# Kernel tuning notes

Measured on AMD Instinct MI355X. Metric: run time of the kernel, lower is better.

Reference implementation:

```python
import jax, jax.numpy as jnp
import numpy as np


def setup_inputs() -> dict:
    key = jax.random.key(0)
    kq, kk, kv = jax.random.split(key, 3)
    B, N, D = 16, 2048, 64
    queries = jax.random.normal(kq, (B, N, D), dtype=jnp.float32)
    keys = jax.random.normal(kk, (B, N, D), dtype=jnp.float32)
    values = jax.random.normal(kv, (B, N, D), dtype=jnp.float32)
    return {"queries": queries, "keys": keys, "values": values}


def reference(queries, keys, values):
    d = queries.shape[-1]
    scale = 1.0 / jnp.sqrt(jnp.asarray(d, dtype=queries.dtype))
    # scores: [B, Nq, Nk]
    scores = jnp.einsum("bqd,bkd->bqk", queries, keys) * scale
    # Faithful to the original: softmax over dim=0 (the batch dimension).
    attn = jax.nn.softmax(scores, axis=0)
    # dropout p=0.0 -> identity
    return jnp.einsum("bqk,bkd->bqd", attn, values)
```

## Files before the change

### kernel.cpp

```cpp
#include <hip/hip_runtime.h>
#include <hip/hip_bf16.h>

typedef __attribute__((ext_vector_type(8))) short short8;
typedef __attribute__((ext_vector_type(4))) short short4v;
typedef __attribute__((ext_vector_type(2))) int   int2v;
typedef __attribute__((ext_vector_type(4))) float floatx4;

#define BATCH 16
#define SEQ   2048
#define DIM   64
#define QSCALE 0.18033688011112042f
#define WS_NEED (12u*1024u*1024u)

__device__ __forceinline__ unsigned short f2bf(float f) {
    return __builtin_bit_cast(unsigned short, __float2bfloat16(f));
}

#if defined(__has_builtin)
#if __has_builtin(__builtin_amdgcn_exp2f)
#define EXP2(x) __builtin_amdgcn_exp2f(x)
#endif
#endif
#ifndef EXP2
#define EXP2(x) exp2f(x)
#endif

#if defined(__has_builtin)
#if __has_builtin(__builtin_amdgcn_mfma_f32_16x16x16bf16_1k)
#define MFMA16(A,B,C) __builtin_amdgcn_mfma_f32_16x16x16bf16_1k(A,B,C,0,0,0)
#elif __has_builtin(__builtin_amdgcn_mfma_f32_16x16x16_bf16)
#define MFMA16(A,B,C) __builtin_amdgcn_mfma_f32_16x16x16_bf16(A,B,C,0,0,0)
#endif
#endif
#ifndef MFMA16
__device__ __forceinline__ floatx4 mfma16_asm(short4v a, short4v b, floatx4 c) {
    asm volatile("s_nop 1\n\tv_mfma_f32_16x16x16_bf16 %0, %1, %2, %0"
                 : "+v"(c) : "v"(a), "v"(b));
    return c;
}
#define MFMA16(A,B,C) mfma16_asm(A,B,C)
#endif

__global__ __launch_bounds__(256)
void convert_kernel(const float* __restrict__ Q, const float* __restrict__ K,
                    const float* __restrict__ V, unsigned short* __restrict__ ws) {
    const int t = blockIdx.x * 256 + threadIdx.x;
    if (t < 524288) {
        const int region = t >> 18;
        const int r = t & 262143;
        const int b = r >> 14;
        const int rem = r & 16383;
        const int t16 = rem >> 7;
        const int st  = (rem >> 6) & 1;
        const int l   = rem & 63;
        const int a = l & 15, g = l >> 4;
        const float* src = (region == 0 ? Q : K) +
            ((size_t)(b * SEQ + t16 * 16 + a)) * DIM + st * 32 + g * 8;
        const float s = (region == 0) ? QSCALE : 1.0f;
        short8 o;
        #pragma unroll
        for (int p = 0; p < 8; ++p) o[p] = (short)f2bf(src[p] * s);
        *(short8*)(ws + (size_t)region * 2097152 + (size_t)r * 8) = o;
    } else {
        const int r = t - 524288;
        const int b  = r >> 13;
        const int kt = (r >> 6) & 127;
        const int l  = r & 63;
        const int a = l & 15, g = l >> 4;
        const float* src = V + ((size_t)(b * SEQ + kt * 16 + g * 4)) * DIM + a;
        short8 o0, o1;
        #pragma unroll
        for (int dt = 0; dt < 2; ++dt)
            #pragma unroll
            for (int p = 0; p < 4; ++p)
                o0[dt * 4 + p] = (short)f2bf(src[(size_t)p * DIM + dt * 16]);
        #pragma unroll
        for (int dt = 2; dt < 4; ++dt)
            #pragma unroll
            for (int p = 0; p < 4; ++p)
                o1[(dt - 2) * 4 + p] = (short)f2bf(src[(size_t)p * DIM + dt * 16]);
        unsigned short* dst = ws + 4194304 + (size_t)r * 16;
        *(short8*)(dst)     = o0;
        *(short8*)(dst + 8) = o1;
    }
}

__global__ __launch_bounds__(512)
void dpa_main(const unsigned short* __restrict__ Qw, const unsigned short* __restrict__ Kw,
              const unsigned short* __restrict__ Vw, float* __restrict__ Og) {
    __shared__ __align__(16) float dl[2][4][64][8];

    const int tid = threadIdx.x;
    const int l = tid & 63;
    const int w = tid >> 6;
    const int a = l & 15, g = l >> 4;
    const int bx = blockIdx.x;
    const int ch = bx & 3;
    const int qt = bx >> 2;
    const int b0 = w * 2;
    const int wsw = w ^ (l >> 3);

    const unsigned short* Kb = Kw + (size_t)b0 * 131072 + l * 8;
    const unsigned short* Vb = Vw + (size_t)b0 * 131072 + l * 16;

    short8 Qf[2][2];
    {
        const unsigned short* Qb = Qw + (size_t)b0 * 131072 + qt * 1024 + l * 8;
        #pragma unroll
        for (int bb = 0; bb < 2; ++bb)
            #pragma unroll
            for (int st = 0; st < 2; ++st)
                Qf[bb][st] = *(const short8*)(Qb + bb * 131072 + st * 512);
    }

    short8 Kf[2][2];
    #pragma unroll
    for (int bb = 0; bb < 2; ++bb)
        #pragma unroll
        for (int st = 0; st < 2; ++st)
            Kf[bb][st] = *(const short8*)(Kb + bb * 131072 + (ch * 32) * 1024 + st * 512);

    floatx4 O[2][4];
    #pragma unroll
    for (int bb = 0; bb < 2; ++bb)
        #pragma unroll
        for (int dt = 0; dt < 4; ++dt) O[bb][dt] = (floatx4)0.0f;

    #pragma unroll 2
    for (int it = 0; it < 32; ++it) {
        const int buf = it & 1;
        const int kt = ch * 32 + it;

        floatx4 S[2];
        __builtin_amdgcn_s_setprio(1);
        #pragma unroll
        for (int bb = 0; bb < 2; ++bb) {
            floatx4 s = (floatx4)0.0f;
            s = __builtin_amdgcn_mfma_f32_16x16x32_bf16(Kf[bb][0], Qf[bb][0], s, 0, 0, 0);
            s = __builtin_amdgcn_mfma_f32_16x16x32_bf16(Kf[bb][1], Qf[bb][1], s, 0, 0, 0);
            S[bb] = s;
        }
        __builtin_amdgcn_s_setprio(0);

        const int ktn = (it < 31) ? (kt + 1) : kt;
        #pragma unroll
        for (int bb = 0; bb < 2; ++bb)
            #pragma unroll
            for (int st = 0; st < 2; ++st)
                Kf[bb][st] = *(const short8*)(Kb + bb * 131072 + ktn * 1024 + st * 512);

        short8 V01[2], V23[2];
        #pragma unroll
        for (int bb = 0; bb < 2; ++bb) {
            const unsigned short* vp = Vb + bb * 131072 + kt * 1024;
            V01[bb] = *(const short8*)(vp);
            V23[bb] = *(const short8*)(vp + 8);
        }

        #pragma unroll
        for (int r = 0; r < 4; ++r) {
            float e0 = EXP2(S[0][r]);
            float e1 = EXP2(S[1][r]);
            S[0][r] = e0; S[1][r] = e1;
            dl[buf][r][l][wsw] = e0 + e1;
        }
        __syncthreads();

        float fr[4];
        #pragma unroll
        for (int r = 0; r < 4; ++r) {
            const floatx4 t0 = *(const floatx4*)&dl[buf][r][l][0];
            const floatx4 t1 = *(const floatx4*)&dl[buf][r][l][4];
            const floatx4 ts = t0 + t1;
            fr[r] = __builtin_amdgcn_rcpf((ts[0] + ts[1]) + (ts[2] + ts[3]));
        }

        #pragma unroll
        for (int bb = 0; bb < 2; ++bb) {
            const unsigned int c0 = __builtin_bit_cast(unsigned int, S[bb][0] * fr[0]) + 0x8000u;
            const unsigned int c1 = __builtin_bit_cast(unsigned int, S[bb][1] * fr[1]) + 0x8000u;
            const unsigned int c2 = __builtin_bit_cast(unsigned int, S[bb][2] * fr[2]) + 0x8000u;
            const unsigned int c3 = __builtin_bit_cast(unsigned int, S[bb][3] * fr[3]) + 0x8000u;
            int2v pp;
            pp[0] = (int)__builtin_amdgcn_perm(c1, c0, 0x07060302u);
            pp[1] = (int)__builtin_amdgcn_perm(c3, c2, 0x07060302u);
            const short4v af = __builtin_bit_cast(short4v, pp);

            const short4v vb0 = __builtin_shufflevector(V01[bb], V01[bb], 0, 1, 2, 3);
            const short4v vb1 = __builtin_shufflevector(V01[bb], V01[bb], 4, 5, 6, 7);
            const short4v vb2 = __builtin_shufflevector(V23[bb], V23[bb], 0, 1, 2, 3);
            const short4v vb3 = __builtin_shufflevector(V23[bb], V23[bb], 4, 5, 6, 7);

            __builtin_amdgcn_s_setprio(1);
            O[bb][0] = MFMA16(af, vb0, O[bb][0]);
            O[bb][1] = MFMA16(af, vb1, O[bb][1]);
            O[bb][2] = MFMA16(af, vb2, O[bb][2]);
            O[bb][3] = MFMA16(af, vb3, O[bb][3]);
            __builtin_amdgcn_s_setprio(0);
        }
    }

    asm volatile("s_nop 7\n\ts_nop 7" :::);

    #pragma unroll
    for (int bb = 0; bb < 2; ++bb)
        #pragma unroll
        for (int dt = 0; dt < 4; ++dt)
            #pragma unroll
            for (int r = 0; r < 4; ++r)
                unsafeAtomicAdd(Og + ((size_t)((b0 + bb) * SEQ + qt * 16 + g * 4 + r)) * DIM
                                    + dt * 16 + a,
                                O[bb][dt][r]);
}

__global__ __launch_bounds__(512)
void dpa_naive(const float* __restrict__ Q, const float* __restrict__ K,
               const float* __restrict__ V, float* __restrict__ out) {
    __shared__ float attn_lds[BATCH][8][64];
    const int tid = threadIdx.x;
    const int lane_k = tid & 63, row_q = tid >> 6, lane_d = tid & 63;
    const int q0 = blockIdx.x * 8;
    float acc[BATCH];
    #pragma unroll
    for (int b = 0; b < BATCH; ++b) acc[b] = 0.0f;
    for (int k0 = 0; k0 < SEQ; k0 += 64) {
        float s[BATCH];
        #pragma unroll
        for (int b = 0; b < BATCH; ++b) {
            const float4* qrow = (const float4*)(Q + ((size_t)b * SEQ + (q0 + row_q)) * DIM);
            const float4* krow = (const float4*)(K + ((size_t)b * SEQ + (k0 + lane_k)) * DIM);
            float a0 = 0.f;
            #pragma unroll
            for (int d4 = 0; d4 < 16; ++d4) {
                float4 qa = qrow[d4]; float4 kb = krow[d4];
                a0 += qa.x*kb.x + qa.y*kb.y + qa.z*kb.z + qa.w*kb.w;
            }
            s[b] = a0 * 0.125f;
        }
        float m = s[0];
        #pragma unroll
        for (int b = 1; b < BATCH; ++b) m = fmaxf(m, s[b]);
        float den = 0.f;
        #pragma unroll
        for (int b = 0; b < BATCH; ++b) { s[b] = __expf(s[b] - m); den += s[b]; }
        const float inv = 1.0f / den;
        #pragma unroll
        for (int b = 0; b < BATCH; ++b) attn_lds[b][row_q][lane_k] = s[b] * inv;
        __syncthreads();
        #pragma unroll
        for (int b = 0; b < BATCH; ++b) {
            const float* vbase = V + ((size_t)b * SEQ + k0) * DIM + lane_d;
            float acc2 = 0.f;
            #pragma unroll 8
            for (int kk = 0; kk < 64; ++kk) acc2 += attn_lds[b][row_q][kk] * vbase[(size_t)kk * DIM];
            acc[b] += acc2;
        }
        __syncthreads();
    }
    #pragma unroll
    for (int b = 0; b < BATCH; ++b)
        out[((size_t)b * SEQ + (q0 + row_q)) * DIM + lane_d] = acc[b];
}

extern "C" void kernel_launch(void* const* d_in, const int* in_sizes, int n_in,
                              void* d_out, int out_size, void* d_ws, size_t ws_size,
                              hipStream_t stream) {
    const float* Q = (const float*)d_in[0];
    const float* K = (const float*)d_in[1];
    const float* V = (const float*)d_in[2];
    float* out = (float*)d_out;

    if (ws_size < WS_NEED) {
        dpa_naive<<<dim3(SEQ / 8), dim3(512), 0, stream>>>(Q, K, V, out);
        return;
    }
    unsigned short* ws = (unsigned short*)d_ws;
    hipMemsetAsync(d_out, 0, (size_t)out_size * sizeof(float), stream);
    convert_kernel<<<dim3(2560), dim3(256), 0, stream>>>(Q, K, V, ws);
    dpa_main<<<dim3(512), dim3(512), 0, stream>>>(ws, ws + 2097152, ws + 4194304, out);
}
```

Baseline: 81.93 us.

## Software-pipeline QK/exp of next key tile with PV of previous tile

Restructures the main attention loop into a skewed pipeline. Each step computes QK scores and exponentials for key tile T while the batch-softmax normalisation and PV MFMAs for tile T-1 run in the same step, with tile T-1's V loads issued early. The aim is to hide MFMA and exp latency behind each other and give the V loads more time to land. In exchange the loop now needs two __syncthreads per iteration instead of one to protect the double-buffered LDS partial sums. The LDS row stride is also padded from 8 to 12 floats, which is meant to reduce bank conflicts.

Result: no change. 82.31 us (+0.5%).

```diff
diff --git a/kernel.cpp b/kernel.cpp
--- a/kernel.cpp
+++ b/kernel.cpp
@@ -24,6 +24,8 @@
 #ifndef EXP2
 #define EXP2(x) exp2f(x)
 #endif
+
+#define MFMA32(A,B,C) __builtin_amdgcn_mfma_f32_16x16x32_bf16(A,B,C,0,0,0)
 
 #if defined(__has_builtin)
 #if __has_builtin(__builtin_amdgcn_mfma_f32_16x16x16bf16_1k)
@@ -88,7 +90,7 @@
 __global__ __launch_bounds__(512)
 void dpa_main(const unsigned short* __restrict__ Qw, const unsigned short* __restrict__ Kw,
               const unsigned short* __restrict__ Vw, float* __restrict__ Og) {
-    __shared__ __align__(16) float dl[2][4][64][8];
+    __shared__ __align__(16) float dl[2][4][64][12];
 
     const int tid = threadIdx.x;
     const int l = tid & 63;
@@ -126,78 +128,103 @@
         #pragma unroll
         for (int dt = 0; dt < 4; ++dt) O[bb][dt] = (floatx4)0.0f;
 
-    #pragma unroll 2
-    for (int it = 0; it < 32; ++it) {
-        const int buf = it & 1;
-        const int kt = ch * 32 + it;
-
-        floatx4 S[2];
-        __builtin_amdgcn_s_setprio(1);
-        #pragma unroll
-        for (int bb = 0; bb < 2; ++bb) {
-            floatx4 s = (floatx4)0.0f;
-            s = __builtin_amdgcn_mfma_f32_16x16x32_bf16(Kf[bb][0], Qf[bb][0], s, 0, 0, 0);
-            s = __builtin_amdgcn_mfma_f32_16x16x32_bf16(Kf[bb][1], Qf[bb][1], s, 0, 0, 0);
-            S[bb] = s;
-        }
-        __builtin_amdgcn_s_setprio(0);
-
-        const int ktn = (it < 31) ? (kt + 1) : kt;
-        #pragma unroll
-        for (int bb = 0; bb < 2; ++bb)
-            #pragma unroll
-            for (int st = 0; st < 2; ++st)
-                Kf[bb][st] = *(const short8*)(Kb + bb * 131072 + ktn * 1024 + st * 512);
-
-        short8 V01[2], V23[2];
-        #pragma unroll
-        for (int bb = 0; bb < 2; ++bb) {
-            const unsigned short* vp = Vb + bb * 131072 + kt * 1024;
-            V01[bb] = *(const short8*)(vp);
-            V23[bb] = *(const short8*)(vp + 8);
-        }
-
-        #pragma unroll
-        for (int r = 0; r < 4; ++r) {
-            float e0 = EXP2(S[0][r]);
-            float e1 = EXP2(S[1][r]);
-            S[0][r] = e0; S[1][r] = e1;
-            dl[buf][r][l][wsw] = e0 + e1;
-        }
-        __syncthreads();
-
-        float fr[4];
-        #pragma unroll
-        for (int r = 0; r < 4; ++r) {
-            const floatx4 t0 = *(const floatx4*)&dl[buf][r][l][0];
-            const floatx4 t1 = *(const floatx4*)&dl[buf][r][l][4];
-            const floatx4 ts = t0 + t1;
-            fr[r] = __builtin_amdgcn_rcpf((ts[0] + ts[1]) + (ts[2] + ts[3]));
-        }
-
-        #pragma unroll
-        for (int bb = 0; bb < 2; ++bb) {
-            const unsigned int c0 = __builtin_bit_cast(unsigned int, S[bb][0] * fr[0]) + 0x8000u;
-            const unsigned int c1 = __builtin_bit_cast(unsigned int, S[bb][1] * fr[1]) + 0x8000u;
-            const unsigned int c2 = __builtin_bit_cast(unsigned int, S[bb][2] * fr[2]) + 0x8000u;
-            const unsigned int c3 = __builtin_bit_cast(unsigned int, S[bb][3] * fr[3]) + 0x8000u;
-            int2v pp;
-            pp[0] = (int)__builtin_amdgcn_perm(c1, c0, 0x07060302u);
-            pp[1] = (int)__builtin_amdgcn_perm(c3, c2, 0x07060302u);
-            const short4v af = __builtin_bit_cast(short4v, pp);
-
-            const short4v vb0 = __builtin_shufflevector(V01[bb], V01[bb], 0, 1, 2, 3);
-            const short4v vb1 = __builtin_shufflevector(V01[bb], V01[bb], 4, 5, 6, 7);
-            const short4v vb2 = __builtin_shufflevector(V23[bb], V23[bb], 0, 1, 2, 3);
-            const short4v vb3 = __builtin_shufflevector(V23[bb], V23[bb], 4, 5, 6, 7);
-
-            __builtin_amdgcn_s_setprio(1);
-            O[bb][0] = MFMA16(af, vb0, O[bb][0]);
-            O[bb][1] = MFMA16(af, vb1, O[bb][1]);
-            O[bb][2] = MFMA16(af, vb2, O[bb][2]);
-            O[bb][3] = MFMA16(af, vb3, O[bb][3]);
-            __builtin_amdgcn_s_setprio(0);
-        }
+    floatx4 SA[2], SB[2];
+
+#define QKEXP(T, SOUT)                                                        \
+    __builtin_amdgcn_s_setprio(1);                                            \
+    {                                                                         \
+        floatx4 s0 = (floatx4)0.0f, s1 = (floatx4)0.0f;                       \
+        s0 = MFMA32(Kf[0][0], Qf[0][0], s0);                                  \
+        s0 = MFMA32(Kf[0][1], Qf[0][1], s0);                                  \
+        s1 = MFMA32(Kf[1][0], Qf[1][0], s1);                                  \
+        s1 = MFMA32(Kf[1][1], Qf[1][1], s1);                                  \
+        SOUT[0] = s0; SOUT[1] = s1;                                           \
+    }                                                                         \
+    __builtin_amdgcn_s_setprio(0);                                            \
+    {                                                                         \
+        const int ktn_ = ch * 32 + (((T) < 31) ? (T) + 1 : 31);               \
+        Kf[0][0] = *(const short8*)(Kb + 0 * 131072 + ktn_ * 1024);           \
+        Kf[0][1] = *(const short8*)(Kb + 0 * 131072 + ktn_ * 1024 + 512);     \
+        Kf[1][0] = *(const short8*)(Kb + 1 * 131072 + ktn_ * 1024);           \
+        Kf[1][1] = *(const short8*)(Kb + 1 * 131072 + ktn_ * 1024 + 512);     \
+    }                                                                         \
+    _Pragma("unroll")                                                         \
+    for (int r = 0; r < 4; ++r) {                                             \
+        const float e0 = EXP2(SOUT[0][r]);                                    \
+        const float e1 = EXP2(SOUT[1][r]);                                    \
+        SOUT[0][r] = e0; SOUT[1][r] = e1;                                     \
+        dl[(T) & 1][r][l][wsw] = e0 + e1;                                     \
+    }
+
+#define COMBINE_PV(T, SPREV, v01_0, v23_0, v01_1, v23_1)                      \
+    {                                                                         \
+        float fr_[4];                                                         \
+        _Pragma("unroll")                                                     \
+        for (int r = 0; r < 4; ++r) {                                         \
+            const floatx4 u0 = *(const floatx4*)&dl[((T)-1) & 1][r][l][0];    \
+            const floatx4 u1 = *(const floatx4*)&dl[((T)-1) & 1][r][l][4];    \
+            const floatx4 us = u0 + u1;                                       \
+            fr_[r] = __builtin_amdgcn_rcpf((us[0] + us[1]) + (us[2] + us[3]));\
+        }                                                                     \
+        _Pragma("unroll")                                                     \
+        for (int bb = 0; bb < 2; ++bb) {                                      \
+            const short8 v01 = (bb == 0) ? v01_0 : v01_1;                     \
+            const short8 v23 = (bb == 0) ? v23_0 : v23_1;                     \
+            const unsigned int c0 = __builtin_bit_cast(unsigned int, SPREV[bb][0] * fr_[0]) + 0x8000u; \
+            const unsigned int c1 = __builtin_bit_cast(unsigned int, SPREV[bb][1] * fr_[1]) + 0x8000u; \
+            const unsigned int c2 = __builtin_bit_cast(unsigned int, SPREV[bb][2] * fr_[2]) + 0x8000u; \
+            const unsigned int c3 = __builtin_bit_cast(unsigned int, SPREV[bb][3] * fr_[3]) + 0x8000u; \
+            int2v pp;                                                         \
+            pp[0] = (int)__builtin_amdgcn_perm(c1, c0, 0x07060302u);          \
+            pp[1] = (int)__builtin_amdgcn_perm(c3, c2, 0x07060302u);          \
+            const short4v af = __builtin_bit_cast(short4v, pp);               \
+            const short4v b0v = __builtin_shufflevector(v01, v01, 0, 1, 2, 3);\
+            const short4v b1v = __builtin_shufflevector(v01, v01, 4, 5, 6, 7);\
+            const short4v b2v = __builtin_shufflevector(v23, v23, 0, 1, 2, 3);\
+            const short4v b3v = __builtin_shufflevector(v23, v23, 4, 5, 6, 7);\
+            __builtin_amdgcn_s_setprio(1);                                    \
+            O[bb][0] = MFMA16(af, b0v, O[bb][0]);                             \
+            O[bb][1] = MFMA16(af, b1v, O[bb][1]);                             \
+            O[bb][2] = MFMA16(af, b2v, O[bb][2]);                             \
+            O[bb][3] = MFMA16(af, b3v, O[bb][3]);                             \
+            __builtin_amdgcn_s_setprio(0);                                    \
+        }                                                                     \
+    }
+
+#define BODY(T, SOUT, SPREV)                                                  \
+    {                                                                         \
+        const int ktp_ = ch * 32 + (T) - 1;                                   \
+        const unsigned short* vp0_ = Vb + 0 * 131072 + ktp_ * 1024;           \
+        const unsigned short* vp1_ = Vb + 1 * 131072 + ktp_ * 1024;           \
+        const short8 V01_0_ = *(const short8*)(vp0_);                         \
+        const short8 V23_0_ = *(const short8*)(vp0_ + 8);                     \
+        const short8 V01_1_ = *(const short8*)(vp1_);                         \
+        const short8 V23_1_ = *(const short8*)(vp1_ + 8);                     \
+        QKEXP(T, SOUT)                                                        \
+        __syncthreads();                                                      \
+        COMBINE_PV(T, SPREV, V01_0_, V23_0_, V01_1_, V23_1_)                  \
+        __syncthreads();                                                      \
+    }
+
+    QKEXP(0, SA)
+
+    #pragma unroll 1
+    for (int j = 0; j < 15; ++j) {
+        const int t1 = 2 * j + 1;
+        BODY(t1, SB, SA)
+        BODY(t1 + 1, SA, SB)
+    }
+    BODY(31, SB, SA)
+
+    {
+        const int ktp = ch * 32 + 31;
+        const unsigned short* vp0 = Vb + 0 * 131072 + ktp * 1024;
+        const unsigned short* vp1 = Vb + 1 * 131072 + ktp * 1024;
+        const short8 V01_0 = *(const short8*)(vp0);
+        const short8 V23_0 = *(const short8*)(vp0 + 8);
+        const short8 V01_1 = *(const short8*)(vp1);
+        const short8 V23_1 = *(const short8*)(vp1 + 8);
+        COMBINE_PV(32, SB, V01_0, V23_0, V01_1, V23_1)
     }
 
     asm volatile("s_nop 7\n\ts_nop 7" :::);
@@ -211,6 +238,9 @@
                 unsafeAtomicAdd(Og + ((size_t)((b0 + bb) * SEQ + qt * 16 + g * 4 + r)) * DIM
                                     + dt * 16 + a,
                                 O[bb][dt][r]);
+#undef BODY
+#undef COMBINE_PV
+#undef QKEXP
 }
 
 __global__ __launch_bounds__(512)
```
